# Kernel optimization log

Measured on AMD Instinct MI355X. Metric: run time of the kernel, lower is better.

## Reference

```python
import jax, jax.numpy as jnp
import numpy as np

THRESHOLD = 0.5
NEG_POS_RATIO = 3


def cxcycz_to_xyz(c):
    return jnp.concatenate([c[..., :3] - c[..., 3:] / 2, c[..., :3] + c[..., 3:] / 2], axis=-1)


def xyz_to_cxcycz(x):
    return jnp.concatenate([(x[..., :3] + x[..., 3:]) / 2, x[..., 3:] - x[..., :3]], axis=-1)


def cxcycz_to_gcxgcygcz(c, priors):
    # SSD offset encoding (variance 0.1 / 0.2), 3D version
    return jnp.concatenate([
        (c[..., :3] - priors[..., :3]) / (priors[..., 3:] / 10.0),
        jnp.log(c[..., 3:] / priors[..., 3:]) * 5.0,
    ], axis=-1)


def jaccard3d(a, b):
    # a: [n,6] xyz boxes, b: [m,6] xyz boxes -> [n,m] IoU
    lo = jnp.maximum(a[:, None, :3], b[None, :, :3])
    hi = jnp.minimum(a[:, None, 3:], b[None, :, 3:])
    inter = jnp.prod(jnp.clip(hi - lo, 0.0, None), axis=-1)
    va = jnp.prod(a[:, 3:] - a[:, :3], axis=-1)
    vb = jnp.prod(b[:, 3:] - b[:, :3], axis=-1)
    return inter / (va[:, None] + vb[None, :] - inter)


def setup_inputs() -> dict:
    key = jax.random.key(0)
    ks = jax.random.split(key, 6)
    B, P, n_obj, n_classes = 16, 131072, 16, 2
    predicted_locs = jax.random.normal(ks[0], (B, P, 6), jnp.float32)
    predicted_scores = jax.random.normal(ks[1], (B, P, n_classes), jnp.float32)
    ctr = jax.random.uniform(ks[2], (B, n_obj, 3), minval=0.2, maxval=0.8)
    sz = jax.random.uniform(ks[3], (B, n_obj, 3), minval=0.05, maxval=0.2)
    boxes = jnp.concatenate([ctr - sz / 2, ctr + sz / 2], axis=-1)
    labels = jnp.ones((B, n_obj), jnp.int32)  # single foreground class (lesion)
    pctr = jax.random.uniform(ks[4], (P, 3), minval=0.0, maxval=1.0)
    psz = jax.random.uniform(ks[5], (P, 3), minval=0.05, maxval=0.3)
    priors_cxcycz = jnp.concatenate([pctr, psz], axis=-1)
    return {
        'predicted_locs': predicted_locs,
        'predicted_scores': predicted_scores,
        'boxes': boxes,
        'labels': labels,
        'priors_cxcycz': priors_cxcycz,
    }


def reference(predicted_locs, predicted_scores, boxes, labels, priors_cxcycz):
    B, P, n_classes = predicted_scores.shape
    n_obj = boxes.shape[1]
    priors_xyz = cxcycz_to_xyz(priors_cxcycz)

    def match(boxes_i, labels_i):
        ov = jaccard3d(boxes_i, priors_xyz)              # [n_obj, P]
        overlap_fp = ov.max(axis=0)                      # best overlap per prior
        object_fp = jnp.argmax(ov, axis=0)               # best object per prior
        prior_fo = jnp.argmax(ov, axis=1)                # best prior per object
        # force each object's best prior to be matched to that object
        object_fp = object_fp.at[prior_fo].set(jnp.arange(n_obj))
        overlap_fp = overlap_fp.at[prior_fo].set(1.0)
        lab = jnp.where(overlap_fp < THRESHOLD, 0, labels_i[object_fp])
        tl = cxcycz_to_gcxgcygcz(xyz_to_cxcycz(boxes_i[object_fp]), priors_cxcycz)
        return lab, tl

    true_classes, true_locs = jax.vmap(match)(boxes, labels)  # [B,P], [B,P,6]

    pos = true_classes > 0                               # [B,P]
    n_pos = pos.sum(axis=1)                              # [B]
    total_pos = n_pos.sum()

    # L1Loss(mean) over positive rows of [*,6]
    loc_abs = jnp.abs(predicted_locs - true_locs).sum(axis=-1)   # [B,P]
    loc_loss = (loc_abs * pos).sum() / (total_pos * 6).astype(predicted_locs.dtype)

    # per-prior cross-entropy
    logp = jax.nn.log_softmax(predicted_scores, axis=-1)
    conf_all = -jnp.take_along_axis(logp, true_classes[..., None], axis=-1)[..., 0]
    conf_all = jnp.where(true_classes < 0, 0.0, conf_all)  # ignored priors (soft mode only)
    conf_pos_sum = (conf_all * pos).sum()

    # hard-negative mining: zero out positives, sort each row descending, take top 3*n_pos
    conf_neg = jnp.where(pos, 0.0, conf_all)
    conf_neg_sorted = -jnp.sort(-conf_neg, axis=1)
    hard = jnp.arange(P)[None, :] < (NEG_POS_RATIO * n_pos)[:, None]
    conf_loss = (jnp.where(hard, conf_neg_sorted, 0.0).sum() + conf_pos_sum) / total_pos.astype(predicted_scores.dtype)
    return conf_loss, loc_loss
```

## Files before the change

kernel.cpp:

```cpp
#include <hip/hip_runtime.h>
#include <math.h>

#define MITEMS 2
#define TILE 512
#define LB 32


__device__ __forceinline__ unsigned long long umax64(unsigned long long a,
                                                     unsigned long long b) {
  return a > b ? a : b;
}

template <int NOBJ, bool FULL>
__global__ __launch_bounds__(256) void mbl_match(
    const float* __restrict__ boxes, const float* __restrict__ priors,
    unsigned long long* __restrict__ prior_fo, unsigned char* __restrict__ best_u8,
    int P, int n_obj) {
  const int b = blockIdx.y;
  const int tid = threadIdx.x;
  __shared__ float4 s_box[NOBJ][2];
  __shared__ unsigned s_iou[8][264];
  __shared__ unsigned s_pinv[8][264];
  for (int i = tid; i < NOBJ; i += 256) {
    float4 v0, v1;
    if (i < n_obj) {
      const float* bx = boxes + ((size_t)b * n_obj + i) * 6;
      const float l0 = bx[0], l1 = bx[1], l2 = bx[2];
      const float h0 = bx[3], h1 = bx[4], h2 = bx[5];
      v0 = make_float4(l0, l1, l2, h0);
      v1 = make_float4(h1, h2, ((h0 - l0) * (h1 - l1)) * (h2 - l2), 0.f);
    } else {
      v0 = make_float4(3e18f, 3e18f, 3e18f, 1e18f);
      v1 = make_float4(1e18f, 1e18f, 0.f, 0.f);
    }
    s_box[i][0] = v0;
    s_box[i][1] = v1;
  }
  __syncthreads();

  const int pbase = blockIdx.x * TILE;
  float lo0[MITEMS], lo1[MITEMS], lo2[MITEMS], hi0[MITEMS], hi1[MITEMS],
      hi2[MITEMS], vb[MITEMS];
  unsigned invp[MITEMS];
#pragma unroll
  for (int k = 0; k < MITEMS; ++k) {
    const int p = pbase + k * 256 + tid;
    if (FULL || p < P) {
      const float2 q0 = *(const float2*)(priors + (size_t)p * 6);
      const float2 q1 = *(const float2*)(priors + (size_t)p * 6 + 2);
      const float2 q2 = *(const float2*)(priors + (size_t)p * 6 + 4);
      lo0[k] = q0.x - q1.y * 0.5f; hi0[k] = q0.x + q1.y * 0.5f;
      lo1[k] = q0.y - q2.x * 0.5f; hi1[k] = q0.y + q2.x * 0.5f;
      lo2[k] = q1.x - q2.y * 0.5f; hi2[k] = q1.x + q2.y * 0.5f;
      vb[k] = (q1.y * q2.x) * q2.y;
      invp[k] = 0xFFFFFFFFu - (unsigned)p;
    } else {
      lo0[k] = lo1[k] = lo2[k] = 3e18f;
      hi0[k] = hi1[k] = hi2[k] = 3e18f;
      vb[k] = 0.f;
      invp[k] = 0u;
    }
  }

  float bv[MITEMS];
  int bo[MITEMS];
#pragma unroll
  for (int k = 0; k < MITEMS; ++k) { bv[k] = -1.0f; bo[k] = 0; }

  for (int pass = 0; pass < NOBJ / 8; ++pass) {
    if (pass) __syncthreads();
    float piou[8];
    unsigned pinv[8];
#pragma unroll
    for (int oo = 0; oo < 8; ++oo) { piou[oo] = 0.f; pinv[oo] = 0u; }

#pragma unroll
    for (int oo = 0; oo < 8; ++oo) {
      const int o = pass * 8 + oo;
      const float4 c0 = s_box[o][0];
      const float4 c1 = s_box[o][1];
#pragma unroll
      for (int k = 0; k < MITEMS; ++k) {
        const float d0 = fminf(c0.w, hi0[k]) - fmaxf(c0.x, lo0[k]);
        const float d1 = fminf(c1.x, hi1[k]) - fmaxf(c0.y, lo1[k]);
        const float d2 = fminf(c1.y, hi2[k]) - fmaxf(c0.z, lo2[k]);
        const float inter = (fmaxf(d0, 0.f) * fmaxf(d1, 0.f)) * fmaxf(d2, 0.f);
        const float un = (c1.z + vb[k]) - inter;
        const float iou = inter * __builtin_amdgcn_rcpf(un);
        if (iou > bv[k]) { bv[k] = iou; bo[k] = o; }
        const bool win = iou > piou[oo];
        piou[oo] = win ? iou : piou[oo];
        pinv[oo] = win ? invp[k] : pinv[oo];
      }
    }

#pragma unroll
    for (int oo = 0; oo < 8; ++oo) {
      s_iou[oo][tid] = __float_as_uint(piou[oo]);
      s_pinv[oo][tid] = pinv[oo];
    }
    __syncthreads();
    const int obj8 = tid >> 5, j = tid & 31;
    unsigned long long m = 0ULL;
#pragma unroll
    for (int i = 0; i < 8; ++i) {
      const int col = j + 32 * i;
      m = umax64(m, ((unsigned long long)s_iou[obj8][col] << 32) |
                        s_pinv[obj8][col]);
    }
#pragma unroll
    for (int off = 1; off < 32; off <<= 1)
      m = umax64(m, __shfl_xor(m, off, 64));
    if (j == 0) {
      const int o = pass * 8 + obj8;
      if (o < n_obj) atomicMax(&prior_fo[(size_t)b * 64 + o], m);
    }
  }

#pragma unroll
  for (int k = 0; k < MITEMS; ++k) {
    const int p = pbase + k * 256 + tid;
    if (FULL || p < P)
      best_u8[(size_t)b * P + p] =
          (unsigned char)((unsigned)bo[k] | (bv[k] >= 0.5f ? 0x80u : 0u));
  }
}

template <int CC>
__global__ __launch_bounds__(256) void mbl_loss(
    const float* __restrict__ locs, const float* __restrict__ scores,
    const float* __restrict__ boxes, const int* __restrict__ labels,
    const float* __restrict__ priors, const unsigned long long* __restrict__ prior_fo,
    const unsigned char* __restrict__ best_u8, float* __restrict__ conf_neg,
    unsigned* __restrict__ hist0, int* __restrict__ n_pos,
    double* __restrict__ pconf, double* __restrict__ ploc, int P, int n_obj,
    int C) {
  const int b = blockIdx.y;
  const int tid = threadIdx.x;
  __shared__ float s_box[64][6];
  __shared__ int s_lab[64];
  __shared__ unsigned s_fo[64];
  __shared__ unsigned s_hist[4096];
  for (int i = tid; i < 4096; i += 256) s_hist[i] = 0u;
  for (int i = tid; i < n_obj * 6; i += 256)
    s_box[i / 6][i % 6] = boxes[(size_t)b * n_obj * 6 + i];
  for (int i = tid; i < n_obj; i += 256) {
    s_lab[i] = labels[(size_t)b * n_obj + i];
    s_fo[i] = 0xFFFFFFFFu - (unsigned)(prior_fo[(size_t)b * 64 + i] & 0xFFFFFFFFull);
  }
  __syncthreads();

  unsigned fo_r[16];
  const bool small_obj = (n_obj <= 16);
  if (small_obj) {
#pragma unroll
    for (int o = 0; o < 16; ++o) fo_r[o] = (o < n_obj) ? s_fo[o] : 0xFFFFFFFEu;
  }

  int np_l = 0;
  double cf_l = 0.0, lc_l = 0.0;

  if (CC == 2 && (P & 1) == 0) {
    const int P2 = P >> 1;
    const int chunk = (P2 + (int)gridDim.x - 1) / (int)gridDim.x;
    const int start = blockIdx.x * chunk;
    const int end = min(start + chunk, P2);
    for (int q = start + tid; q < end; q += 256) {
      const float4 sc = *(const float4*)(scores + ((size_t)b * P2 + q) * 4);
      const unsigned short bpp =
          *(const unsigned short*)(best_u8 + (size_t)b * P + 2 * q);
      float cn2[2];
#pragma unroll
      for (int e = 0; e < 2; ++e) {
        const int p = 2 * q + e;
        const unsigned bp = e ? (bpp >> 8) : (bpp & 0xFFu);
        int obj = bp & 0x7F;
        int posf = (int)(bp >> 7);
        if (small_obj) {
#pragma unroll
          for (int o = 0; o < 16; ++o)
            if (fo_r[o] == (unsigned)p) { obj = o; posf = 1; }
        } else {
          for (int o = 0; o < n_obj; ++o)
            if (s_fo[o] == (unsigned)p) { obj = o; posf = 1; }
        }
        const int lab = posf ? s_lab[obj] : 0;
        const float sx = e ? sc.z : sc.x;
        const float sy = e ? sc.w : sc.y;
        const float mm = fmaxf(sx, sy);
        const float conf =
            (lab < 0) ? 0.f
                      : (mm + __logf(__expf(sx - mm) + __expf(sy - mm)) -
                         ((lab == 0) ? sx : sy));
        float cn = conf;
        if (lab > 0) {
          np_l++;
          cf_l += (double)conf;
          const float* pr = priors + (size_t)p * 6;
          const float* pl = locs + ((size_t)b * P + p) * 6;
          float ls = 0.f;
          for (int i = 0; i < 3; ++i) {
            const float c0 = (s_box[obj][i] + s_box[obj][i + 3]) * 0.5f;
            const float szb = s_box[obj][i + 3] - s_box[obj][i];
            const float g = (c0 - pr[i]) / (pr[i + 3] / 10.0f);
            const float g2 = logf(szb / pr[i + 3]) * 5.0f;
            ls += fabsf(pl[i] - g) + fabsf(pl[i + 3] - g2);
          }
          lc_l += (double)ls;
          cn = 0.f;
        }
        cn2[e] = cn;
        atomicAdd(&s_hist[__float_as_uint(cn) >> 20], 1u);
      }
      *(float2*)(conf_neg + (size_t)b * P + 2 * q) = make_float2(cn2[0], cn2[1]);
    }
  } else {
    const int chunk = (P + (int)gridDim.x - 1) / (int)gridDim.x;
    const int start = blockIdx.x * chunk;
    const int end = min(start + chunk, P);
    for (int p = start + tid; p < end; p += 256) {
      const unsigned char bp = best_u8[(size_t)b * P + p];
      int obj = bp & 0x7F;
      int posf = bp >> 7;
      for (int o = 0; o < n_obj; ++o)
        if (s_fo[o] == (unsigned)p) { obj = o; posf = 1; }
      const int lab = posf ? s_lab[obj] : 0;
      const float* sp = scores + ((size_t)b * P + p) * C;
      float m = sp[0];
      for (int c = 1; c < C; ++c) m = fmaxf(m, sp[c]);
      float se = 0.f;
      for (int c = 0; c < C; ++c) se += __expf(sp[c] - m);
      const float conf = (lab < 0) ? 0.f : (m + __logf(se) - sp[lab]);
      float cn = conf;
      if (lab > 0) {
        np_l++;
        cf_l += (double)conf;
        const float* pr = priors + (size_t)p * 6;
        const float* pl = locs + ((size_t)b * P + p) * 6;
        float ls = 0.f;
        for (int i = 0; i < 3; ++i) {
          const float c0 = (s_box[obj][i] + s_box[obj][i + 3]) * 0.5f;
          const float szb = s_box[obj][i + 3] - s_box[obj][i];
          const float g = (c0 - pr[i]) / (pr[i + 3] / 10.0f);
          const float g2 = logf(szb / pr[i + 3]) * 5.0f;
          ls += fabsf(pl[i] - g) + fabsf(pl[i + 3] - g2);
        }
        lc_l += (double)ls;
        cn = 0.f;
      }
      conf_neg[(size_t)b * P + p] = cn;
      atomicAdd(&s_hist[__float_as_uint(cn) >> 20], 1u);
    }
  }

  __shared__ int r_np[256];
  __shared__ double r_c[256];
  __shared__ double r_l[256];
  r_np[tid] = np_l;
  r_c[tid] = cf_l;
  r_l[tid] = lc_l;
  __syncthreads();
  for (int s = 128; s > 0; s >>= 1) {
    if (tid < s) {
      r_np[tid] += r_np[tid + s];
      r_c[tid] += r_c[tid + s];
      r_l[tid] += r_l[tid + s];
    }
    __syncthreads();
  }
  if (tid == 0 && r_np[0] > 0) {
    atomicAdd(&n_pos[b], r_np[0]);
    atomicAdd(&pconf[b], r_c[0]);
    atomicAdd(&ploc[b], r_l[0]);
  }
  for (int i = tid; i < 4096; i += 256)
    if (s_hist[i]) atomicAdd(&hist0[(size_t)b * 4096 + i], s_hist[i]);
}

template <int BINS>
__device__ void block_select(const unsigned* __restrict__ h, int remk,
                             unsigned* s_scan, int* s_out, unsigned* sel,
                             int* remk_o) {
  constexpr int BPT = BINS / 256;
  const int t = threadIdx.x;
  if (t == 0) { s_out[0] = BINS - 1; s_out[1] = 0; }
  unsigned mb[BPT];
  unsigned s = 0;
#pragma unroll
  for (int i = 0; i < BPT; ++i) { mb[i] = h[t * BPT + i]; s += mb[i]; }
  unsigned incl = s;
  s_scan[t] = incl;
  __syncthreads();
  for (int off = 1; off < 256; off <<= 1) {
    const unsigned add = (t >= off) ? s_scan[t - off] : 0u;
    __syncthreads();
    incl += add;
    s_scan[t] = incl;
    __syncthreads();
  }
  const unsigned total = s_scan[255];
  const unsigned R = total - incl;
  if (remk > 0 && R < (unsigned)remk && R + s >= (unsigned)remk) {
    unsigned acc = R;
    int sel_i = t * BPT, rk = 0;
    bool done = false;
#pragma unroll
    for (int i = BPT - 1; i >= 0; --i) {
      if (!done && acc + mb[i] >= (unsigned)remk) {
        sel_i = t * BPT + i;
        rk = remk - (int)acc;
        done = true;
      }
      if (!done) acc += mb[i];
    }
    s_out[0] = sel_i;
    s_out[1] = rk;
  }
  __syncthreads();
  *sel = (unsigned)s_out[0];
  *remk_o = s_out[1];
  __syncthreads();
}

__global__ __launch_bounds__(256) void mbl_hist1(
    const float* __restrict__ conf_neg, const int* __restrict__ n_pos,
    const unsigned* __restrict__ hist0, unsigned* __restrict__ hist1, int P) {
  const int b = blockIdx.y;
  const int tid = threadIdx.x;
  __shared__ unsigned s_scan[256];
  __shared__ int s_out[2];
  __shared__ unsigned s_hist[4096];
  int K = 3 * n_pos[b];
  if (K > P) K = P;
  unsigned sel0;
  int rem0;
  block_select<4096>(hist0 + (size_t)b * 4096, K, s_scan, s_out, &sel0, &rem0);
  for (int i = tid; i < 4096; i += 256) s_hist[i] = 0u;
  __syncthreads();
  const float* row = conf_neg + (size_t)b * P;
  const int n4 = P >> 2;
  const int per = (n4 + (int)gridDim.x - 1) / (int)gridDim.x;
  const int s4 = blockIdx.x * per, e4 = min(s4 + per, n4);
  for (int i = s4 + tid; i < e4; i += 256) {
    const float4 v = ((const float4*)row)[i];
    unsigned u;
    u = __float_as_uint(v.x); if ((u >> 20) == sel0) atomicAdd(&s_hist[(u >> 8) & 4095u], 1u);
    u = __float_as_uint(v.y); if ((u >> 20) == sel0) atomicAdd(&s_hist[(u >> 8) & 4095u], 1u);
    u = __float_as_uint(v.z); if ((u >> 20) == sel0) atomicAdd(&s_hist[(u >> 8) & 4095u], 1u);
    u = __float_as_uint(v.w); if ((u >> 20) == sel0) atomicAdd(&s_hist[(u >> 8) & 4095u], 1u);
  }
  if (blockIdx.x == 0)
    for (int p = (n4 << 2) + tid; p < P; p += 256) {
      const unsigned u = __float_as_uint(row[p]);
      if ((u >> 20) == sel0) atomicAdd(&s_hist[(u >> 8) & 4095u], 1u);
    }
  __syncthreads();
  for (int i = tid; i < 4096; i += 256)
    if (s_hist[i]) atomicAdd(&hist1[(size_t)b * 4096 + i], s_hist[i]);
}

__global__ __launch_bounds__(256) void mbl_sum(
    const float* __restrict__ conf_neg, const int* __restrict__ n_pos,
    const unsigned* __restrict__ hist0, const unsigned* __restrict__ hist1,
    const double* __restrict__ pconf, const double* __restrict__ ploc,
    double* __restrict__ phard, unsigned* __restrict__ counter, int P, int B,
    float* __restrict__ out) {
  const int b = blockIdx.y;
  const int tid = threadIdx.x;
  __shared__ unsigned s_scan[256];
  __shared__ int s_out[2];
  int K = 3 * n_pos[b];
  if (K > P) K = P;
  unsigned sel0, sel1;
  int rem0, rem1;
  block_select<4096>(hist0 + (size_t)b * 4096, K, s_scan, s_out, &sel0, &rem0);
  block_select<4096>(hist1 + (size_t)b * 4096, rem0, s_scan, s_out, &sel1, &rem1);
  const unsigned pref24 = (sel0 << 12) | sel1;
  const unsigned tb = (pref24 << 8) | 0xFFu;
  const float* row = conf_neg + (size_t)b * P;
  const int n4 = P >> 2;
  const int per = (n4 + (int)gridDim.x - 1) / (int)gridDim.x;
  const int s4 = blockIdx.x * per, e4 = min(s4 + per, n4);
  double local = 0.0;
  for (int i = s4 + tid; i < e4; i += 256) {
    const float4 v = ((const float4*)row)[i];
    if (__float_as_uint(v.x) > tb) local += (double)v.x;
    if (__float_as_uint(v.y) > tb) local += (double)v.y;
    if (__float_as_uint(v.z) > tb) local += (double)v.z;
    if (__float_as_uint(v.w) > tb) local += (double)v.w;
  }
  if (blockIdx.x == 0) {
    for (int p = (n4 << 2) + tid; p < P; p += 256) {
      const float v = row[p];
      if (__float_as_uint(v) > tb) local += (double)v;
    }
    if (tid == 0 && rem1 > 0)
      local += (double)rem1 * (double)__uint_as_float((pref24 << 8) | 0x80u);
  }
  __shared__ double red[256];
  red[tid] = local;
  __syncthreads();
  for (int s = 128; s > 0; s >>= 1) {
    if (tid < s) red[tid] += red[tid + s];
    __syncthreads();
  }
  if (tid == 0) {
    if (red[0] != 0.0) atomicAdd(&phard[b], red[0]);
    __threadfence();
    const unsigned done = atomicAdd(counter, 1u);
    if (done == gridDim.x * gridDim.y - 1) {
      double tp = 0.0, cs = 0.0, ls = 0.0, hs = 0.0;
      for (int i = 0; i < B; ++i) {
        tp += (double)n_pos[i];
        cs += pconf[i];
        ls += ploc[i];
        hs += atomicAdd(&phard[i], 0.0);
      }
      out[0] = (float)((hs + cs) / tp);
      out[1] = (float)(ls / (tp * 6.0));
    }
  }
}

extern "C" void kernel_launch(void* const* d_in, const int* in_sizes, int n_in,
                              void* d_out, int out_size, void* d_ws, size_t ws_size,
                              hipStream_t stream) {
  const float* locs = (const float*)d_in[0];
  const float* scores = (const float*)d_in[1];
  const float* boxes = (const float*)d_in[2];
  const int* labels = (const int*)d_in[3];
  const float* priors = (const float*)d_in[4];

  const long long sz_locs = (long long)in_sizes[0];
  const long long sz_scores = (long long)in_sizes[1];
  const long long sz_priors = (long long)in_sizes[4];
  const int P = (int)(sz_priors / 6);
  const int B = (int)(sz_locs / sz_priors);
  const int n_obj = in_sizes[3] / B;
  const int C = (int)(sz_scores * 6 / sz_locs);

  char* ws = (char*)d_ws;
  size_t off = 0;
  double* pconf = (double*)(ws + off); off += (size_t)B * 8;
  double* ploc = (double*)(ws + off); off += (size_t)B * 8;
  double* phard = (double*)(ws + off); off += (size_t)B * 8;
  int* n_pos = (int*)(ws + off); off += ((size_t)B * 4 + 15) & ~(size_t)15;
  unsigned* counter = (unsigned*)(ws + off); off += 16;
  unsigned long long* prior_fo = (unsigned long long*)(ws + off);
  off += (size_t)B * 64 * 8;
  unsigned* hist0 = (unsigned*)(ws + off); off += (size_t)B * 4096 * 4;
  unsigned* hist1 = (unsigned*)(ws + off); off += (size_t)B * 4096 * 4;
  const size_t zero_bytes = off;
  float* conf_neg = (float*)(ws + off); off += ((size_t)B * P * 4 + 15) & ~(size_t)15;
  unsigned char* best_u8 = (unsigned char*)(ws + off);
  off += ((size_t)B * P + 15) & ~(size_t)15;
  (void)ws_size;

  hipMemsetAsync(d_ws, 0, zero_bytes, stream);

  const int nblk = (P + TILE - 1) / TILE;
  const dim3 mgrid(nblk, B);
  const bool full = (P % TILE) == 0;
  if (n_obj <= 16) {
    if (full) mbl_match<16, true><<<mgrid, 256, 0, stream>>>(boxes, priors, prior_fo, best_u8, P, n_obj);
    else      mbl_match<16, false><<<mgrid, 256, 0, stream>>>(boxes, priors, prior_fo, best_u8, P, n_obj);
  } else if (n_obj <= 32) {
    if (full) mbl_match<32, true><<<mgrid, 256, 0, stream>>>(boxes, priors, prior_fo, best_u8, P, n_obj);
    else      mbl_match<32, false><<<mgrid, 256, 0, stream>>>(boxes, priors, prior_fo, best_u8, P, n_obj);
  } else {
    if (full) mbl_match<64, true><<<mgrid, 256, 0, stream>>>(boxes, priors, prior_fo, best_u8, P, n_obj);
    else      mbl_match<64, false><<<mgrid, 256, 0, stream>>>(boxes, priors, prior_fo, best_u8, P, n_obj);
  }

  const dim3 lgrid(LB, B);
  if (C == 2)
    mbl_loss<2><<<lgrid, 256, 0, stream>>>(locs, scores, boxes, labels, priors,
                                           prior_fo, best_u8, conf_neg, hist0, n_pos,
                                           pconf, ploc, P, n_obj, C);
  else
    mbl_loss<0><<<lgrid, 256, 0, stream>>>(locs, scores, boxes, labels, priors,
                                           prior_fo, best_u8, conf_neg, hist0, n_pos,
                                           pconf, ploc, P, n_obj, C);

  mbl_hist1<<<lgrid, 256, 0, stream>>>(conf_neg, n_pos, hist0, hist1, P);
  mbl_sum<<<lgrid, 256, 0, stream>>>(conf_neg, n_pos, hist0, hist1, pconf, ploc,
                                     phard, counter, P, B, (float*)d_out);
}
```

Baseline: 92.41 us.

## Spatially bin priors into grid cells and skip non-overlapping objects per wave

Adds three preprocessing kernels that compute a 16^3 cell histogram of prior centres, a prefix scan, a per-batch per-cell object overlap bitmask (using the maximum prior half-extent), and a cell-sorted copy of the priors. The match kernel reads the sorted priors, ORs the cell masks across each wavefront, and skips IoU computation for objects that cannot overlap any prior in the wave. Results are scattered back to the original prior index. The aim is to cut match ALU work, at the cost of three extra launches, global atomics and a scattered byte write. Skipping only pays off if the wave-level masks are sparse, which depends on how large the maximum prior extent is.

```diff
diff --git a/kernel.cpp b/kernel.cpp
--- a/kernel.cpp
+++ b/kernel.cpp
@@ -4,6 +4,8 @@
 #define MITEMS 2
 #define TILE 512
 #define LB 32
+#define G3 16
+#define CELLS 4096
 
 
 __device__ __forceinline__ unsigned long long umax64(unsigned long long a,
@@ -11,11 +13,115 @@
   return a > b ? a : b;
 }
 
-template <int NOBJ, bool FULL>
+__device__ __forceinline__ int cell_of(float cx, float cy, float cz) {
+  int ix = (int)(cx * G3); ix = min(max(ix, 0), G3 - 1);
+  int iy = (int)(cy * G3); iy = min(max(iy, 0), G3 - 1);
+  int iz = (int)(cz * G3); iz = min(max(iz, 0), G3 - 1);
+  return (iz * G3 + iy) * G3 + ix;
+}
+
+__global__ __launch_bounds__(256) void mbl_s1(const float* __restrict__ priors,
+                                              unsigned* __restrict__ cellhist,
+                                              unsigned* __restrict__ maxhalf,
+                                              int P) {
+  const int p = blockIdx.x * 256 + threadIdx.x;
+  if (p >= P) return;
+  const float2 q0 = *(const float2*)(priors + (size_t)p * 6);
+  const float2 q1 = *(const float2*)(priors + (size_t)p * 6 + 2);
+  const float2 q2 = *(const float2*)(priors + (size_t)p * 6 + 4);
+  const float h0 = q1.y * 0.5f, h1 = q2.x * 0.5f, h2 = q2.y * 0.5f;
+  const float e0 = h0 + fmaxf(q0.x - 1.f, 0.f) + fmaxf(-q0.x, 0.f);
+  const float e1 = h1 + fmaxf(q0.y - 1.f, 0.f) + fmaxf(-q0.y, 0.f);
+  const float e2 = h2 + fmaxf(q1.x - 1.f, 0.f) + fmaxf(-q1.x, 0.f);
+  atomicMax(&maxhalf[0], __float_as_uint(fmaxf(e0, 0.f)));
+  atomicMax(&maxhalf[1], __float_as_uint(fmaxf(e1, 0.f)));
+  atomicMax(&maxhalf[2], __float_as_uint(fmaxf(e2, 0.f)));
+  atomicAdd(&cellhist[cell_of(q0.x, q0.y, q1.x)], 1u);
+}
+
+__global__ __launch_bounds__(256) void mbl_s2(
+    const float* __restrict__ boxes, const unsigned* __restrict__ cellhist,
+    unsigned* __restrict__ offs, unsigned* __restrict__ mask32,
+    unsigned long long* __restrict__ prior_fo,
+    const unsigned* __restrict__ maxhalf, int n_obj) {
+  const int t = threadIdx.x;
+  if (blockIdx.x == 0) {
+    __shared__ unsigned s_scan[256];
+    unsigned v[16];
+    unsigned s = 0;
+#pragma unroll
+    for (int i = 0; i < 16; ++i) { v[i] = cellhist[t * 16 + i]; s += v[i]; }
+    unsigned incl = s;
+    s_scan[t] = incl;
+    __syncthreads();
+    for (int off = 1; off < 256; off <<= 1) {
+      const unsigned add = (t >= off) ? s_scan[t - off] : 0u;
+      __syncthreads();
+      incl += add;
+      s_scan[t] = incl;
+      __syncthreads();
+    }
+    unsigned base = incl - s;
+#pragma unroll
+    for (int i = 0; i < 16; ++i) { offs[t * 16 + i] = base; base += v[i]; }
+  } else {
+    const int b = blockIdx.x - 1;
+    __shared__ float s_lo[64][3], s_hi[64][3];
+    if (t < n_obj) {
+      const float* q = boxes + ((size_t)b * n_obj + t) * 6;
+      s_lo[t][0] = q[0]; s_lo[t][1] = q[1]; s_lo[t][2] = q[2];
+      s_hi[t][0] = q[3]; s_hi[t][1] = q[4]; s_hi[t][2] = q[5];
+      prior_fo[(size_t)b * 64 + t] = 0xFFFFFFFFull;
+    }
+    __syncthreads();
+    const float mh0 = __uint_as_float(maxhalf[0]);
+    const float mh1 = __uint_as_float(maxhalf[1]);
+    const float mh2 = __uint_as_float(maxhalf[2]);
+    const int nm = min(n_obj, 32);
+    const float inv = 1.0f / (float)G3;
+    for (int c = t; c < CELLS; c += 256) {
+      const int ix = c & (G3 - 1), iy = (c >> 4) & (G3 - 1), iz = c >> 8;
+      const float clo0 = ix * inv, chi0 = (ix + 1) * inv;
+      const float clo1 = iy * inv, chi1 = (iy + 1) * inv;
+      const float clo2 = iz * inv, chi2 = (iz + 1) * inv;
+      unsigned m = 0u;
+      for (int o = 0; o < nm; ++o) {
+        const bool ov = (s_lo[o][0] - mh0) <= chi0 && (s_hi[o][0] + mh0) >= clo0 &&
+                        (s_lo[o][1] - mh1) <= chi1 && (s_hi[o][1] + mh1) >= clo1 &&
+                        (s_lo[o][2] - mh2) <= chi2 && (s_hi[o][2] + mh2) >= clo2;
+        m |= ov ? (1u << o) : 0u;
+      }
+      mask32[(size_t)b * CELLS + c] = m;
+    }
+  }
+}
+
+__global__ __launch_bounds__(256) void mbl_s3(const float* __restrict__ priors,
+                                              const unsigned* __restrict__ offs,
+                                              unsigned* __restrict__ cellcnt,
+                                              float4* __restrict__ sorted, int P) {
+  const int p = blockIdx.x * 256 + threadIdx.x;
+  if (p >= P) return;
+  const float2 q0 = *(const float2*)(priors + (size_t)p * 6);
+  const float2 q1 = *(const float2*)(priors + (size_t)p * 6 + 2);
+  const float2 q2 = *(const float2*)(priors + (size_t)p * 6 + 4);
+  const float lo0 = q0.x - q1.y * 0.5f, hi0 = q0.x + q1.y * 0.5f;
+  const float lo1 = q0.y - q2.x * 0.5f, hi1 = q0.y + q2.x * 0.5f;
+  const float lo2 = q1.x - q2.y * 0.5f, hi2 = q1.x + q2.y * 0.5f;
+  const float vb = (q1.y * q2.x) * q2.y;
+  const int c = cell_of(q0.x, q0.y, q1.x);
+  const unsigned slot = offs[c] + atomicAdd(&cellcnt[c], 1u);
+  sorted[(size_t)slot * 2] = make_float4(lo0, lo1, lo2, vb);
+  sorted[(size_t)slot * 2 + 1] =
+      make_float4(hi0, hi1, hi2,
+                  __uint_as_float(((unsigned)c << 17) | (unsigned)p));
+}
+
+template <int NOBJ, bool USEMASK>
 __global__ __launch_bounds__(256) void mbl_match(
-    const float* __restrict__ boxes, const float* __restrict__ priors,
-    unsigned long long* __restrict__ prior_fo, unsigned char* __restrict__ best_u8,
-    int P, int n_obj) {
+    const float* __restrict__ boxes, const float4* __restrict__ sorted,
+    const unsigned* __restrict__ mask32, unsigned long long* __restrict__ prior_fo,
+    unsigned char* __restrict__ best_u8, int P, int n_obj) {
   const int b = blockIdx.y;
   const int tid = threadIdx.x;
   __shared__ float4 s_box[NOBJ][2];
@@ -41,31 +147,40 @@
   const int pbase = blockIdx.x * TILE;
   float lo0[MITEMS], lo1[MITEMS], lo2[MITEMS], hi0[MITEMS], hi1[MITEMS],
       hi2[MITEMS], vb[MITEMS];
-  unsigned invp[MITEMS];
+  unsigned invp[MITEMS], origp[MITEMS], lmk[MITEMS];
 #pragma unroll
   for (int k = 0; k < MITEMS; ++k) {
-    const int p = pbase + k * 256 + tid;
-    if (FULL || p < P) {
-      const float2 q0 = *(const float2*)(priors + (size_t)p * 6);
-      const float2 q1 = *(const float2*)(priors + (size_t)p * 6 + 2);
-      const float2 q2 = *(const float2*)(priors + (size_t)p * 6 + 4);
-      lo0[k] = q0.x - q1.y * 0.5f; hi0[k] = q0.x + q1.y * 0.5f;
-      lo1[k] = q0.y - q2.x * 0.5f; hi1[k] = q0.y + q2.x * 0.5f;
-      lo2[k] = q1.x - q2.y * 0.5f; hi2[k] = q1.x + q2.y * 0.5f;
-      vb[k] = (q1.y * q2.x) * q2.y;
-      invp[k] = 0xFFFFFFFFu - (unsigned)p;
+    const int slot = pbase + k * 256 + tid;
+    if (slot < P) {
+      const float4 r0 = sorted[(size_t)slot * 2];
+      const float4 r1 = sorted[(size_t)slot * 2 + 1];
+      lo0[k] = r0.x; lo1[k] = r0.y; lo2[k] = r0.z; vb[k] = r0.w;
+      hi0[k] = r1.x; hi1[k] = r1.y; hi2[k] = r1.z;
+      const unsigned pkd = __float_as_uint(r1.w);
+      const unsigned cell = pkd >> 17;
+      origp[k] = pkd & 0x1FFFFu;
+      invp[k] = 0xFFFFFFFFu - origp[k];
+      lmk[k] = USEMASK ? mask32[(size_t)b * CELLS + cell] : 0xFFFFFFFFu;
     } else {
       lo0[k] = lo1[k] = lo2[k] = 3e18f;
       hi0[k] = hi1[k] = hi2[k] = 3e18f;
       vb[k] = 0.f;
       invp[k] = 0u;
-    }
-  }
+      origp[k] = 0xFFFFFFFFu;
+      lmk[k] = 0u;
+    }
+  }
+
+  unsigned lm = lmk[0] | lmk[1];
+#pragma unroll
+  for (int off = 1; off < 64; off <<= 1) lm |= __shfl_xor(lm, off, 64);
+  const unsigned umask =
+      USEMASK ? __builtin_amdgcn_readfirstlane(lm) : 0xFFFFFFFFu;
 
   float bv[MITEMS];
   int bo[MITEMS];
 #pragma unroll
-  for (int k = 0; k < MITEMS; ++k) { bv[k] = -1.0f; bo[k] = 0; }
+  for (int k = 0; k < MITEMS; ++k) { bv[k] = 0.0f; bo[k] = 0; }
 
   for (int pass = 0; pass < NOBJ / 8; ++pass) {
     if (pass) __syncthreads();
@@ -73,24 +188,27 @@
     unsigned pinv[8];
 #pragma unroll
     for (int oo = 0; oo < 8; ++oo) { piou[oo] = 0.f; pinv[oo] = 0u; }
+    const unsigned upass = (umask >> (pass * 8)) & 0xFFu;
 
 #pragma unroll
     for (int oo = 0; oo < 8; ++oo) {
-      const int o = pass * 8 + oo;
-      const float4 c0 = s_box[o][0];
-      const float4 c1 = s_box[o][1];
-#pragma unroll
-      for (int k = 0; k < MITEMS; ++k) {
-        const float d0 = fminf(c0.w, hi0[k]) - fmaxf(c0.x, lo0[k]);
-        const float d1 = fminf(c1.x, hi1[k]) - fmaxf(c0.y, lo1[k]);
-        const float d2 = fminf(c1.y, hi2[k]) - fmaxf(c0.z, lo2[k]);
-        const float inter = (fmaxf(d0, 0.f) * fmaxf(d1, 0.f)) * fmaxf(d2, 0.f);
-        const float un = (c1.z + vb[k]) - inter;
-        const float iou = inter * __builtin_amdgcn_rcpf(un);
-        if (iou > bv[k]) { bv[k] = iou; bo[k] = o; }
-        const bool win = iou > piou[oo];
-        piou[oo] = win ? iou : piou[oo];
-        pinv[oo] = win ? invp[k] : pinv[oo];
+      if (upass & (1u << oo)) {
+        const int o = pass * 8 + oo;
+        const float4 c0 = s_box[o][0];
+        const float4 c1 = s_box[o][1];
+#pragma unroll
+        for (int k = 0; k < MITEMS; ++k) {
+          const float d0 = fminf(c0.w, hi0[k]) - fmaxf(c0.x, lo0[k]);
+          const float d1 = fminf(c1.x, hi1[k]) - fmaxf(c0.y, lo1[k]);
+          const float d2 = fminf(c1.y, hi2[k]) - fmaxf(c0.z, lo2[k]);
+          const float inter = (fmaxf(d0, 0.f) * fmaxf(d1, 0.f)) * fmaxf(d2, 0.f);
+          const float un = (c1.z + vb[k]) - inter;
+          const float iou = inter * __builtin_amdgcn_rcpf(un);
+          if (iou > bv[k]) { bv[k] = iou; bo[k] = o; }
+          const bool win = iou > piou[oo];
+          piou[oo] = win ? iou : piou[oo];
+          pinv[oo] = win ? invp[k] : pinv[oo];
+        }
       }
     }
 
@@ -119,9 +237,9 @@
 
 #pragma unroll
   for (int k = 0; k < MITEMS; ++k) {
-    const int p = pbase + k * 256 + tid;
-    if (FULL || p < P)
-      best_u8[(size_t)b * P + p] =
+    const int slot = pbase + k * 256 + tid;
+    if (slot < P)
+      best_u8[(size_t)b * P + origp[k]] =
           (unsigned char)((unsigned)bo[k] | (bv[k] >= 0.5f ? 0x80u : 0u));
   }
 }
@@ -450,26 +568,38 @@
   off += (size_t)B * 64 * 8;
   unsigned* hist0 = (unsigned*)(ws + off); off += (size_t)B * 4096 * 4;
   unsigned* hist1 = (unsigned*)(ws + off); off += (size_t)B * 4096 * 4;
+  unsigned* cellhist = (unsigned*)(ws + off); off += (size_t)CELLS * 4;
+  unsigned* cellcnt = (unsigned*)(ws + off); off += (size_t)CELLS * 4;
+  unsigned* maxhalf = (unsigned*)(ws + off); off += 16;
   const size_t zero_bytes = off;
+  unsigned* offs = (unsigned*)(ws + off); off += (size_t)CELLS * 4;
+  unsigned* mask32 = (unsigned*)(ws + off); off += (size_t)B * CELLS * 4;
   float* conf_neg = (float*)(ws + off); off += ((size_t)B * P * 4 + 15) & ~(size_t)15;
   unsigned char* best_u8 = (unsigned char*)(ws + off);
   off += ((size_t)B * P + 15) & ~(size_t)15;
+  off = (off + 15) & ~(size_t)15;
+  float4* sorted = (float4*)(ws + off); off += (size_t)P * 2 * 16;
   (void)ws_size;
 
   hipMemsetAsync(d_ws, 0, zero_bytes, stream);
+
+  const int pblk = (P + 255) / 256;
+  mbl_s1<<<pblk, 256, 0, stream>>>(priors, cellhist, maxhalf, P);
+  mbl_s2<<<1 + B, 256, 0, stream>>>(boxes, cellhist, offs, mask32, prior_fo,
+                                    maxhalf, n_obj);
+  mbl_s3<<<pblk, 256, 0, stream>>>(priors, offs, cellcnt, sorted, P);
 
   const int nblk = (P + TILE - 1) / TILE;
   const dim3 mgrid(nblk, B);
-  const bool full = (P % TILE) == 0;
   if (n_obj <= 16) {
-    if (full) mbl_match<16, true><<<mgrid, 256, 0, stream>>>(boxes, priors, prior_fo, best_u8, P, n_obj);
-    else      mbl_match<16, false><<<mgrid, 256, 0, stream>>>(boxes, priors, prior_fo, best_u8, P, n_obj);
+    mbl_match<16, true><<<mgrid, 256, 0, stream>>>(boxes, sorted, mask32,
+                                                   prior_fo, best_u8, P, n_obj);
   } else if (n_obj <= 32) {
-    if (full) mbl_match<32, true><<<mgrid, 256, 0, stream>>>(boxes, priors, prior_fo, best_u8, P, n_obj);
-    else      mbl_match<32, false><<<mgrid, 256, 0, stream>>>(boxes, priors, prior_fo, best_u8, P, n_obj);
+    mbl_match<32, true><<<mgrid, 256, 0, stream>>>(boxes, sorted, mask32,
+                                                   prior_fo, best_u8, P, n_obj);
   } else {
-    if (full) mbl_match<64, true><<<mgrid, 256, 0, stream>>>(boxes, priors, prior_fo, best_u8, P, n_obj);
-    else      mbl_match<64, false><<<mgrid, 256, 0, stream>>>(boxes, priors, prior_fo, best_u8, P, n_obj);
+    mbl_match<64, false><<<mgrid, 256, 0, stream>>>(boxes, sorted, mask32,
+                                                    prior_fo, best_u8, P, n_obj);
   }
 
   const dim3 lgrid(LB, B);
```

New measurement: 221.1 us. +139.2%, slower.
